# Performance work log

Measured on AMD Instinct MI355X. Metric: run time of the kernel, lower is better.

The kernel has to match this reference:

```python
import jax, jax.numpy as jnp
import numpy as np

N = 50000
E = 400000
IN_DIM = 256
H1 = 512
H2 = 128
P_DROP = 0.5


def setup_inputs() -> dict:
    key = jax.random.key(0)
    ks = jax.random.split(key, 8)
    x = jax.random.normal(ks[0], (N, IN_DIM), dtype=jnp.float32)
    edge_index = jax.random.randint(ks[1], (2, E), 0, N, dtype=jnp.int64)
    W1 = jax.random.normal(ks[2], (IN_DIM, H1), dtype=jnp.float32) * (1.0 / np.sqrt(IN_DIM))
    b1 = jnp.zeros((H1,), dtype=jnp.float32)
    W2 = jax.random.normal(ks[3], (H1, H2), dtype=jnp.float32) * (1.0 / np.sqrt(H1))
    b2 = jnp.zeros((H2,), dtype=jnp.float32)
    a = jnp.full((1,), 0.25, dtype=jnp.float32)  # PReLU default init
    mask1 = jax.random.bernoulli(ks[4], 1.0 - P_DROP, (N, H1))
    mask2 = jax.random.bernoulli(ks[5], 1.0 - P_DROP, (N, H2))
    return {"x": x, "edge_index": edge_index, "W1": W1, "b1": b1,
            "W2": W2, "b2": b2, "a": a, "mask1": mask1, "mask2": mask2}


def reference(x, edge_index, W1, b1, W2, b2, a, mask1, mask2):
    n = x.shape[0]
    loop = jnp.arange(n, dtype=edge_index.dtype)
    src = jnp.concatenate([edge_index[0], loop])  # [E+N] with self-loops
    dst = jnp.concatenate([edge_index[1], loop])
    # symmetric normalization: deg^-1/2[src] * deg^-1/2[dst]
    deg = jax.ops.segment_sum(jnp.ones(src.shape[0], x.dtype), dst, num_segments=n)
    dis = jnp.where(deg > 0, jax.lax.rsqrt(jnp.maximum(deg, 1.0)), 0.0)
    norm = dis[src] * dis[dst]  # [E+N]

    scale = 1.0 / (1.0 - P_DROP)

    def gcn_conv(h, W, b):
        h = h @ W                               # dense transform [n, out]
        msg = h[src] * norm[:, None]            # gather + normalize [E+N, out]
        return jax.ops.segment_sum(msg, dst, num_segments=n) + b

    def prelu_dropout(h, mask):
        h = jnp.where(h >= 0, h, a * h)         # PReLU (shared scalar a)
        return jnp.where(mask, h * scale, 0.0)  # dropout p=0.5

    feat1 = prelu_dropout(gcn_conv(x, W1, b1), mask1)
    feat2 = prelu_dropout(gcn_conv(feat1, W2, b2), mask2)
    return feat2
```

## Files before the change

kernel.cpp:

```cpp
#include <hip/hip_runtime.h>
#include <hip/hip_bf16.h>

#define IN_DIM 256
#define H1 512
#define H2 128
#define BM 128
#define SCAN_CHUNK 4096

typedef unsigned short u16;
typedef unsigned long long u64;
typedef __attribute__((ext_vector_type(8))) short short8;
typedef __attribute__((ext_vector_type(4))) float floatx4;

__device__ __forceinline__ u16 f2bf(float f) {
    union { float f; unsigned u; } c; c.f = f;
    unsigned u = c.u;
    return (u16)((u + 0x7fffu + ((u >> 16) & 1u)) >> 16);
}
__device__ __forceinline__ float bflo(unsigned w) {
    union { unsigned u; float f; } c; c.u = w << 16; return c.f;
}
__device__ __forceinline__ float bfhi(unsigned w) {
    union { unsigned u; float f; } c; c.u = w & 0xffff0000u; return c.f;
}


__global__ __launch_bounds__(256) void prep_kernel(const int4* __restrict__ mask4,
        u64* __restrict__ bits, int total4,
        const int* __restrict__ dstA, int* __restrict__ counts, int E, int n,
        const float* __restrict__ W1, u16* __restrict__ w1t,
        const float* __restrict__ W2, u16* __restrict__ w2t,
        int PB, int HB, int T1B) {
    int b = blockIdx.x;
    if (b < PB) {
        int gid = b * 256 + threadIdx.x;
        int lane = threadIdx.x & 63;
        int4 v = (gid < total4) ? mask4[gid] : make_int4(0, 0, 0, 0);
        u64 b0 = __ballot(v.x != 0);
        u64 b1 = __ballot(v.y != 0);
        u64 b2 = __ballot(v.z != 0);
        u64 b3 = __ballot(v.w != 0);
        u64 sel = (lane == 0) ? b0 : (lane == 1) ? b1 : (lane == 2) ? b2 : b3;
        if (lane < 4 && gid < total4)
            bits[(size_t)(gid >> 6) * 4 + lane] = sel;
    } else if (b < PB + HB) {
        int e = (b - PB) * 256 + threadIdx.x;
        if (e < E) {
            int d = dstA[e];
            if ((unsigned)d < (unsigned)n) atomicAdd(&counts[d], 1);
        }
    } else if (b < PB + HB + T1B) {
        int idx = (b - PB - HB) * 256 + threadIdx.x;
        if (idx < IN_DIM * H1) {
            int k = idx >> 9, c = idx & (H1 - 1);
            w1t[c * IN_DIM + k] = f2bf(W1[idx]);
        }
    } else {
        int idx = (b - PB - HB - T1B) * 256 + threadIdx.x;
        if (idx < H1 * H2) {
            int k = idx >> 7, c = idx & (H2 - 1);
            w2t[c * H1 + k] = f2bf(W2[idx]);
        }
    }
}


__global__ __launch_bounds__(256) void partial_sum_kernel(const int* __restrict__ counts,
        int* __restrict__ partials, int n) {
    int t = threadIdx.x;
    int base = blockIdx.x * SCAN_CHUNK + t * 16;
    int s = 0;
    int m = (base < n) ? min(16, n - base) : 0;
    for (int i = 0; i < m; ++i) s += (counts[base + i] + 1) & ~1;
    __shared__ int red[256];
    red[t] = s;
    __syncthreads();
    for (int off = 128; off > 0; off >>= 1) {
        if (t < off) red[t] += red[t + off];
        __syncthreads();
    }
    if (t == 0) partials[blockIdx.x] = red[0];
}

__global__ void scan_partials_kernel(int* __restrict__ partials, int nb,
                                     unsigned* __restrict__ ts_zero_row) {
    int t = threadIdx.x;
    if (t < 64) ts_zero_row[t] = 0;
    if (t == 0 && blockIdx.x == 0) {
        int run = 0;
        for (int i = 0; i < nb; ++i) { int c = partials[i]; partials[i] = run; run += c; }
        partials[nb] = run;
    }
}

__global__ __launch_bounds__(256) void scan_emit_kernel(const int* __restrict__ counts,
        const int* __restrict__ partials, int* __restrict__ row_start,
        int* __restrict__ cursor, float* __restrict__ dis,
        int* __restrict__ csr, int n, int nb) {
    int t = threadIdx.x;
    int base = blockIdx.x * SCAN_CHUNK + t * 16;
    int cnt[16];
    int s = 0;
    int m = (base < n) ? min(16, n - base) : 0;
    for (int i = 0; i < m; ++i) { cnt[i] = counts[base + i]; s += (cnt[i] + 1) & ~1; }
    __shared__ int red[256];
    red[t] = s;
    __syncthreads();
    for (int off = 1; off < 256; off <<= 1) {
        int v = red[t];
        int vo = (t >= off) ? red[t - off] : 0;
        __syncthreads();
        red[t] = v + vo;
        __syncthreads();
    }
    int run = partials[blockIdx.x] + (t ? red[t - 1] : 0);
    for (int i = 0; i < m; ++i) {
        int c = cnt[i];
        row_start[base + i] = run;
        cursor[base + i] = run;
        dis[base + i] = rsqrtf((float)(c + 1));
        if (c & 1) csr[run + c] = n;
        run += (c + 1) & ~1;
    }
    if (blockIdx.x == 0 && t == 0) row_start[n] = partials[nb];
}

__global__ void scatter_kernel(const int* __restrict__ srcA, const int* __restrict__ dstA,
                               int* __restrict__ cursor, int* __restrict__ csr,
                               int E, int n) {
    int e = blockIdx.x * blockDim.x + threadIdx.x;
    if (e < E) {
        int d = dstA[e];
        int s = srcA[e];
        if ((unsigned)d < (unsigned)n && (unsigned)s < (unsigned)n) {
            int p = atomicAdd(&cursor[d], 1);
            csr[p] = s;
        }
    }
}

__global__ void scale_cast_kernel(const float* __restrict__ x, const float* __restrict__ dis,
                                  u16* __restrict__ xs, int n) {
    int gid = blockIdx.x * blockDim.x + threadIdx.x;
    int total = (n + 1) * (IN_DIM / 4);
    if (gid >= total) return;
    int node = gid >> 6;
    uint2 o = make_uint2(0, 0);
    if (node < n) {
        float4 v = ((const float4*)x)[gid];
        float d = dis[node];
        o.x = (unsigned)f2bf(v.x * d) | ((unsigned)f2bf(v.y * d) << 16);
        o.y = (unsigned)f2bf(v.z * d) | ((unsigned)f2bf(v.w * d) << 16);
    }
    ((uint2*)xs)[gid] = o;
}


__global__ __launch_bounds__(256) void agg1_kernel(const u16* __restrict__ xs,
        const int* __restrict__ row_start, const int* __restrict__ csr,
        const float* __restrict__ dis, u16* __restrict__ aggx, int n) {
    int gid = blockIdx.x * blockDim.x + threadIdx.x;
    int w = gid >> 6, lane = gid & 63;
    if (w >= n) return;
    const uint4* base = (const uint4*)xs;
    int half = lane >> 5, hl = lane & 31;
    float a0 = 0.f, a1 = 0.f, a2 = 0.f, a3 = 0.f, a4 = 0.f, a5 = 0.f, a6 = 0.f, a7 = 0.f;
    if (half == 0) {
        uint4 u = base[(size_t)w * 32 + hl];
        a0 = bflo(u.x); a1 = bfhi(u.x); a2 = bflo(u.y); a3 = bfhi(u.y);
        a4 = bflo(u.z); a5 = bfhi(u.z); a6 = bflo(u.w); a7 = bfhi(u.w);
    }
    int b = row_start[w], e = row_start[w + 1];
    int i = b;
    for (; i + 8 <= e; i += 8) {
        int s0 = csr[i + half],     s1 = csr[i + 2 + half];
        int s2 = csr[i + 4 + half], s3 = csr[i + 6 + half];
        uint4 u0 = base[(size_t)s0 * 32 + hl];
        uint4 u1 = base[(size_t)s1 * 32 + hl];
        uint4 u2 = base[(size_t)s2 * 32 + hl];
        uint4 u3 = base[(size_t)s3 * 32 + hl];
        a0 += (bflo(u0.x) + bflo(u1.x)) + (bflo(u2.x) + bflo(u3.x));
        a1 += (bfhi(u0.x) + bfhi(u1.x)) + (bfhi(u2.x) + bfhi(u3.x));
        a2 += (bflo(u0.y) + bflo(u1.y)) + (bflo(u2.y) + bflo(u3.y));
        a3 += (bfhi(u0.y) + bfhi(u1.y)) + (bfhi(u2.y) + bfhi(u3.y));
        a4 += (bflo(u0.z) + bflo(u1.z)) + (bflo(u2.z) + bflo(u3.z));
        a5 += (bfhi(u0.z) + bfhi(u1.z)) + (bfhi(u2.z) + bfhi(u3.z));
        a6 += (bflo(u0.w) + bflo(u1.w)) + (bflo(u2.w) + bflo(u3.w));
        a7 += (bfhi(u0.w) + bfhi(u1.w)) + (bfhi(u2.w) + bfhi(u3.w));
    }
    for (; i < e; i += 2) {
        int s = csr[i + half];
        uint4 u = base[(size_t)s * 32 + hl];
        a0 += bflo(u.x); a1 += bfhi(u.x); a2 += bflo(u.y); a3 += bfhi(u.y);
        a4 += bflo(u.z); a5 += bfhi(u.z); a6 += bflo(u.w); a7 += bfhi(u.w);
    }
    a0 += __shfl_xor(a0, 32); a1 += __shfl_xor(a1, 32);
    a2 += __shfl_xor(a2, 32); a3 += __shfl_xor(a3, 32);
    a4 += __shfl_xor(a4, 32); a5 += __shfl_xor(a5, 32);
    a6 += __shfl_xor(a6, 32); a7 += __shfl_xor(a7, 32);
    if (half == 0) {
        float dd = dis[w];
        uint4 o;
        o.x = (unsigned)f2bf(a0 * dd) | ((unsigned)f2bf(a1 * dd) << 16);
        o.y = (unsigned)f2bf(a2 * dd) | ((unsigned)f2bf(a3 * dd) << 16);
        o.z = (unsigned)f2bf(a4 * dd) | ((unsigned)f2bf(a5 * dd) << 16);
        o.w = (unsigned)f2bf(a6 * dd) | ((unsigned)f2bf(a7 * dd) << 16);
        ((uint4*)aggx)[(size_t)w * 32 + hl] = o;
    }
}


__global__ __launch_bounds__(256) void gemm1_kernel(const u16* __restrict__ A,
        const u16* __restrict__ Bt, const float* __restrict__ bias,
        const float* __restrict__ a_p, const u64* __restrict__ mbits,
        u16* __restrict__ out, int M) {
    const int K = IN_DIM;
    __shared__ u64 mb[BM * 5];
    int tid = threadIdx.x;
    int wave = tid >> 6, lane = tid & 63;
    int quad = lane >> 4, l16 = lane & 15;
    int wm = wave & 1, wn = wave >> 1;
    int m0 = blockIdx.x * BM, n0 = blockIdx.y * BM;

    for (int u = tid; u < BM * 4; u += 256) {
        int row = u >> 2, j = u & 3;
        int gr = m0 + row;
        u64 val = 0;
        if (gr < M) val = mbits[(size_t)gr * 8 + (n0 >> 8) * 4 + j];
        mb[row * 5 + j] = val;
    }

    floatx4 acc[4][4];
#pragma unroll
    for (int i = 0; i < 4; i++)
#pragma unroll
        for (int j = 0; j < 4; j++) acc[i][j] = (floatx4){0.f, 0.f, 0.f, 0.f};

    const u16* aptr[4];
#pragma unroll
    for (int mt = 0; mt < 4; mt++) {
        int row = m0 + wm * 64 + mt * 16 + l16;
        if (row >= M) row = M - 1;
        aptr[mt] = A + (size_t)row * K + quad * 8;
    }
    const u16* bptr[4];
#pragma unroll
    for (int i = 0; i < 4; i++)
        bptr[i] = Bt + (size_t)(n0 + wn * 64 + i * 16 + l16) * K + quad * 8;

#pragma unroll
    for (int k0 = 0; k0 < K; k0 += 64) {
        short8 bf[4][2];
#pragma unroll
        for (int i = 0; i < 4; i++) {
            bf[i][0] = *(const short8*)(bptr[i] + k0);
            bf[i][1] = *(const short8*)(bptr[i] + k0 + 32);
        }
#pragma unroll
        for (int mt = 0; mt < 4; mt++) {
            short8 af0 = *(const short8*)(aptr[mt] + k0);
            short8 af1 = *(const short8*)(aptr[mt] + k0 + 32);
#pragma unroll
            for (int nt = 0; nt < 4; nt++) {
                acc[mt][nt] = __builtin_amdgcn_mfma_f32_16x16x32_bf16(
                    af0, bf[nt][0], acc[mt][nt], 0, 0, 0);
                acc[mt][nt] = __builtin_amdgcn_mfma_f32_16x16x32_bf16(
                    af1, bf[nt][1], acc[mt][nt], 0, 0, 0);
            }
        }
    }

    __syncthreads();
    float alpha = a_p[0];
#pragma unroll
    for (int mt = 0; mt < 4; mt++) {
#pragma unroll
        for (int r = 0; r < 4; r++) {
            int lr = wm * 64 + mt * 16 + quad * 4 + r;
            int row = m0 + lr;
            if (row >= M) continue;
#pragma unroll
            for (int nt = 0; nt < 4; nt++) {
                int c64 = nt * 16 + l16;
                int col = n0 + wn * 64 + c64;
                float v = acc[mt][nt][r] + bias[col];
                v = (v >= 0.f) ? v : alpha * v;
                u64 w = mb[lr * 5 + (l16 & 3)];
                int bit = ((n0 >> 2) + wn * 16 + nt * 4 + (l16 >> 2)) & 63;
                v = ((w >> bit) & 1ull) ? v * 2.0f : 0.0f;
                out[(size_t)row * H1 + col] = f2bf(v);
            }
        }
    }
}


__global__ __launch_bounds__(256) void gemm2_kernel(const u16* __restrict__ A,
        const u16* __restrict__ Bt, const float* __restrict__ dis,
        u16* __restrict__ out, int M) {
    const int K = H1;
    int tid = threadIdx.x;
    int wave = tid >> 6, lane = tid & 63;
    int quad = lane >> 4, l16 = lane & 15;
    int wm = wave & 1, wn = wave >> 1;
    int m0 = blockIdx.x * 64;

    floatx4 acc[2][4];
#pragma unroll
    for (int i = 0; i < 2; i++)
#pragma unroll
        for (int j = 0; j < 4; j++) acc[i][j] = (floatx4){0.f, 0.f, 0.f, 0.f};

    const u16* aptr[2];
#pragma unroll
    for (int mt = 0; mt < 2; mt++) {
        int row = m0 + wm * 32 + mt * 16 + l16;
        if (row >= M) row = M - 1;
        aptr[mt] = A + (size_t)row * K + quad * 8;
    }
    const u16* bptr[4];
#pragma unroll
    for (int i = 0; i < 4; i++)
        bptr[i] = Bt + (size_t)(wn * 64 + i * 16 + l16) * K + quad * 8;

#pragma unroll 2
    for (int k0 = 0; k0 < K; k0 += 64) {
        short8 bf[4][2];
#pragma unroll
        for (int i = 0; i < 4; i++) {
            bf[i][0] = *(const short8*)(bptr[i] + k0);
            bf[i][1] = *(const short8*)(bptr[i] + k0 + 32);
        }
#pragma unroll
        for (int mt = 0; mt < 2; mt++) {
            short8 af0 = *(const short8*)(aptr[mt] + k0);
            short8 af1 = *(const short8*)(aptr[mt] + k0 + 32);
#pragma unroll
            for (int nt = 0; nt < 4; nt++) {
                acc[mt][nt] = __builtin_amdgcn_mfma_f32_16x16x32_bf16(
                    af0, bf[nt][0], acc[mt][nt], 0, 0, 0);
                acc[mt][nt] = __builtin_amdgcn_mfma_f32_16x16x32_bf16(
                    af1, bf[nt][1], acc[mt][nt], 0, 0, 0);
            }
        }
    }

#pragma unroll
    for (int mt = 0; mt < 2; mt++) {
#pragma unroll
        for (int r = 0; r < 4; r++) {
            int row = m0 + wm * 32 + mt * 16 + quad * 4 + r;
            if (row >= M) continue;
            float dd = dis[row];
#pragma unroll
            for (int nt = 0; nt < 4; nt++) {
                int col = wn * 64 + nt * 16 + l16;
                out[(size_t)row * H2 + col] = f2bf(acc[mt][nt][r] * dd);
            }
        }
    }
}


__global__ __launch_bounds__(256) void agg2_kernel(const u16* __restrict__ ts,
        const int* __restrict__ row_start, const int* __restrict__ csr,
        const float* __restrict__ dis, const float* __restrict__ b2,
        const float* __restrict__ a_p, const int* __restrict__ mask,
        float* __restrict__ out, int n) {
    int gid = blockIdx.x * blockDim.x + threadIdx.x;
    int w = gid >> 6, lane = gid & 63;
    if (w >= n) return;
    const uint2* base = (const uint2*)ts;
    int half = lane >> 5, hl = lane & 31;
    float a0 = 0.f, a1 = 0.f, a2 = 0.f, a3 = 0.f;
    if (half == 0) {
        uint2 u = base[(size_t)w * 32 + hl];
        a0 = bflo(u.x); a1 = bfhi(u.x); a2 = bflo(u.y); a3 = bfhi(u.y);
    }
    int b = row_start[w], e = row_start[w + 1];
    int i = b;
    for (; i + 8 <= e; i += 8) {
        int s0 = csr[i + half],     s1 = csr[i + 2 + half];
        int s2 = csr[i + 4 + half], s3 = csr[i + 6 + half];
        uint2 u0 = base[(size_t)s0 * 32 + hl];
        uint2 u1 = base[(size_t)s1 * 32 + hl];
        uint2 u2 = base[(size_t)s2 * 32 + hl];
        uint2 u3 = base[(size_t)s3 * 32 + hl];
        a0 += (bflo(u0.x) + bflo(u1.x)) + (bflo(u2.x) + bflo(u3.x));
        a1 += (bfhi(u0.x) + bfhi(u1.x)) + (bfhi(u2.x) + bfhi(u3.x));
        a2 += (bflo(u0.y) + bflo(u1.y)) + (bflo(u2.y) + bflo(u3.y));
        a3 += (bfhi(u0.y) + bfhi(u1.y)) + (bfhi(u2.y) + bfhi(u3.y));
    }
    for (; i < e; i += 2) {
        int s = csr[i + half];
        uint2 u = base[(size_t)s * 32 + hl];
        a0 += bflo(u.x); a1 += bfhi(u.x); a2 += bflo(u.y); a3 += bfhi(u.y);
    }
    a0 += __shfl_xor(a0, 32); a1 += __shfl_xor(a1, 32);
    a2 += __shfl_xor(a2, 32); a3 += __shfl_xor(a3, 32);
    if (half == 0) {
        float dd = dis[w];
        float alpha = a_p[0];
        float4 bb = ((const float4*)b2)[hl];
        float v0 = dd * a0 + bb.x;
        float v1 = dd * a1 + bb.y;
        float v2 = dd * a2 + bb.z;
        float v3 = dd * a3 + bb.w;
        v0 = (v0 >= 0.f) ? v0 : alpha * v0;
        v1 = (v1 >= 0.f) ? v1 : alpha * v1;
        v2 = (v2 >= 0.f) ? v2 : alpha * v2;
        v3 = (v3 >= 0.f) ? v3 : alpha * v3;
        int4 m = ((const int4*)mask)[(size_t)w * 32 + hl];
        v0 = m.x ? v0 * 2.f : 0.f;
        v1 = m.y ? v1 * 2.f : 0.f;
        v2 = m.z ? v2 * 2.f : 0.f;
        v3 = m.w ? v3 * 2.f : 0.f;
        ((float4*)out)[(size_t)w * 32 + hl] = make_float4(v0, v1, v2, v3);
    }
}


extern "C" void kernel_launch(void* const* d_in, const int* in_sizes, int n_in,
                              void* d_out, int out_size, void* d_ws, size_t ws_size,
                              hipStream_t stream) {
    const float* x  = (const float*)d_in[0];
    const int* ei   = (const int*)d_in[1];
    const float* W1 = (const float*)d_in[2];
    const float* b1 = (const float*)d_in[3];
    const float* W2 = (const float*)d_in[4];
    const float* b2 = (const float*)d_in[5];
    const float* ap = (const float*)d_in[6];
    const int* mask1 = (const int*)d_in[7];
    const int* mask2 = (const int*)d_in[8];

    int n = in_sizes[0] / IN_DIM;
    int E = in_sizes[1] / 2;
    const int* srcA = ei;
    const int* dstA = ei + E;

    char* p = (char*)d_ws;
    auto alloc = [&](size_t bytes) {
        char* r = p;
        p += (bytes + 255) & ~(size_t)255;
        return r;
    };
    u16* feat1     = (u16*)alloc((size_t)n * H1 * 2);
    u16* xs        = feat1;
    u16* ts        = (u16*)alloc((size_t)(n + 1) * H2 * 2);
    u64* bits1     = (u64*)ts;
    u16* w1t       = (u16*)alloc((size_t)IN_DIM * H1 * 2);
    u16* w2t       = (u16*)alloc((size_t)H1 * H2 * 2);
    float* dis     = (float*)alloc((size_t)n * 4);
    int* counts    = (int*)alloc((size_t)n * 4);
    int* cursor    = (int*)alloc((size_t)n * 4);
    int* row_start = (int*)alloc(((size_t)n + 1) * 4);
    int* csr       = (int*)alloc(((size_t)E + n + 64) * 4);
    int nscan = (n + SCAN_CHUNK - 1) / SCAN_CHUNK;
    int* partials  = (int*)alloc(((size_t)nscan + 1) * 4);
    u16* aggx      = (u16*)d_out;
    if ((size_t)(p - (char*)d_ws) > ws_size) return;

    const int tpb = 256;
    int total4 = n * H1 / 4;
    int PB = (total4 + tpb - 1) / tpb;
    int HB = (E + tpb - 1) / tpb;
    int T1B = (IN_DIM * H1 + tpb - 1) / tpb;
    int T2B = (H1 * H2 + tpb - 1) / tpb;
    hipMemsetAsync(counts, 0, (size_t)n * 4, stream);
    prep_kernel<<<PB + HB + T1B + T2B, tpb, 0, stream>>>((const int4*)mask1, bits1, total4,
        dstA, counts, E, n, W1, w1t, W2, w2t, PB, HB, T1B);
    partial_sum_kernel<<<nscan, tpb, 0, stream>>>(counts, partials, n);
    scan_partials_kernel<<<1, 64, 0, stream>>>(partials, nscan,
        (unsigned*)(ts + (size_t)n * H2));
    scan_emit_kernel<<<nscan, tpb, 0, stream>>>(counts, partials, row_start, cursor, dis,
                                                csr, n, nscan);
    scatter_kernel<<<(E + tpb - 1) / tpb, tpb, 0, stream>>>(srcA, dstA, cursor, csr, E, n);
    scale_cast_kernel<<<(((n + 1) * (IN_DIM / 4)) + tpb - 1) / tpb, tpb, 0, stream>>>(x, dis, xs, n);
    agg1_kernel<<<(n * 64 + tpb - 1) / tpb, tpb, 0, stream>>>(xs, row_start, csr, dis, aggx, n);
    dim3 g1((n + BM - 1) / BM, H1 / BM);
    gemm1_kernel<<<g1, tpb, 0, stream>>>(aggx, w1t, b1, ap, bits1, feat1, n);
    dim3 g2((n + 63) / 64, 1);
    gemm2_kernel<<<g2, tpb, 0, stream>>>(feat1, w2t, dis, ts, n);
    agg2_kernel<<<(n * 64 + tpb - 1) / tpb, tpb, 0, stream>>>(ts, row_start, csr, dis, b2, ap,
                                                              mask2, (float*)d_out, n);
}
```

Measured before the change: 450.6 us.

## Fuse layer-1 GEMM epilogue with layer-2 GEMM via shared-memory tile

Replaces the separate gemm1 and gemm2 kernels with one kernel per 64-row tile. The aggregated input tile is staged in LDS, the 512-wide hidden layer is computed in two 256-column halves with PReLU and dropout applied, and each half is fed straight into the second GEMM from LDS. This removes the write and re-read of the n×512 bf16 feat1 intermediate and one launch. The cost is lower parallelism (one block per 64 rows), extra syncs, and repeated W1/W2 reads from global memory per block. Buffers are reallocated so the mask bits and xs no longer alias feat1 or ts.

```diff
diff --git a/kernel.cpp b/kernel.cpp
--- a/kernel.cpp
+++ b/kernel.cpp
@@ -4,7 +4,7 @@
 #define IN_DIM 256
 #define H1 512
 #define H2 128
-#define BM 128
+#define LDA 264
 #define SCAN_CHUNK 4096
 
 typedef unsigned short u16;
@@ -210,154 +210,120 @@
 }
 
 
-__global__ __launch_bounds__(256) void gemm1_kernel(const u16* __restrict__ A,
-        const u16* __restrict__ Bt, const float* __restrict__ bias,
+__global__ __launch_bounds__(256) void gemm_fused_kernel(const u16* __restrict__ A,
+        const u16* __restrict__ W1t, const float* __restrict__ b1,
         const float* __restrict__ a_p, const u64* __restrict__ mbits,
-        u16* __restrict__ out, int M) {
-    const int K = IN_DIM;
-    __shared__ u64 mb[BM * 5];
+        const u16* __restrict__ W2t, const float* __restrict__ dis,
+        u16* __restrict__ ts, int M) {
+    __shared__ __align__(16) u16 As[64 * LDA];
+    __shared__ __align__(16) u16 Fs[64 * LDA];
+    __shared__ u64 Mb[64 * 9];
     int tid = threadIdx.x;
     int wave = tid >> 6, lane = tid & 63;
     int quad = lane >> 4, l16 = lane & 15;
-    int wm = wave & 1, wn = wave >> 1;
-    int m0 = blockIdx.x * BM, n0 = blockIdx.y * BM;
-
-    for (int u = tid; u < BM * 4; u += 256) {
-        int row = u >> 2, j = u & 3;
+    int m0 = blockIdx.x * 64;
+
+    for (int u = tid; u < 2048; u += 256) {
+        int row = u >> 5, seg = u & 31;
+        uint4 av = make_uint4(0, 0, 0, 0);
         int gr = m0 + row;
-        u64 val = 0;
-        if (gr < M) val = mbits[(size_t)gr * 8 + (n0 >> 8) * 4 + j];
-        mb[row * 5 + j] = val;
-    }
-
-    floatx4 acc[4][4];
-#pragma unroll
-    for (int i = 0; i < 4; i++)
-#pragma unroll
-        for (int j = 0; j < 4; j++) acc[i][j] = (floatx4){0.f, 0.f, 0.f, 0.f};
-
-    const u16* aptr[4];
-#pragma unroll
-    for (int mt = 0; mt < 4; mt++) {
-        int row = m0 + wm * 64 + mt * 16 + l16;
-        if (row >= M) row = M - 1;
-        aptr[mt] = A + (size_t)row * K + quad * 8;
-    }
-    const u16* bptr[4];
-#pragma unroll
-    for (int i = 0; i < 4; i++)
-        bptr[i] = Bt + (size_t)(n0 + wn * 64 + i * 16 + l16) * K + quad * 8;
-
-#pragma unroll
-    for (int k0 = 0; k0 < K; k0 += 64) {
-        short8 bf[4][2];
-#pragma unroll
-        for (int i = 0; i < 4; i++) {
-            bf[i][0] = *(const short8*)(bptr[i] + k0);
-            bf[i][1] = *(const short8*)(bptr[i] + k0 + 32);
-        }
+        if (gr < M) av = *(const uint4*)&A[(size_t)gr * IN_DIM + seg * 8];
+        *(uint4*)&As[row * LDA + seg * 8] = av;
+    }
+    for (int u = tid; u < 512; u += 256) {
+        int row = u >> 3, j = u & 7;
+        int gr = m0 + row;
+        Mb[row * 9 + j] = (gr < M) ? mbits[(size_t)gr * 8 + j] : 0;
+    }
+    __syncthreads();
+
+    floatx4 acc2[8];
+#pragma unroll
+    for (int i = 0; i < 8; i++) acc2[i] = (floatx4){0.f, 0.f, 0.f, 0.f};
+    float alpha = a_p[0];
+
+#pragma unroll
+    for (int h = 0; h < 2; h++) {
+        floatx4 acc1[4][4];
+#pragma unroll
+        for (int i = 0; i < 4; i++)
+#pragma unroll
+            for (int j = 0; j < 4; j++) acc1[i][j] = (floatx4){0.f, 0.f, 0.f, 0.f};
+        const u16* bptr1[4];
+#pragma unroll
+        for (int nt = 0; nt < 4; nt++)
+            bptr1[nt] = W1t + (size_t)(h * 256 + wave * 64 + nt * 16 + l16) * IN_DIM + quad * 8;
+        float bias_v[4];
+#pragma unroll
+        for (int nt = 0; nt < 4; nt++)
+            bias_v[nt] = b1[h * 256 + wave * 64 + nt * 16 + l16];
+#pragma unroll
+        for (int k0 = 0; k0 < 256; k0 += 64) {
+            short8 bf[4][2], af[4][2];
+#pragma unroll
+            for (int nt = 0; nt < 4; nt++) {
+                bf[nt][0] = *(const short8*)(bptr1[nt] + k0);
+                bf[nt][1] = *(const short8*)(bptr1[nt] + k0 + 32);
+            }
+#pragma unroll
+            for (int mt = 0; mt < 4; mt++) {
+                af[mt][0] = *(const short8*)&As[(mt * 16 + l16) * LDA + k0 + quad * 8];
+                af[mt][1] = *(const short8*)&As[(mt * 16 + l16) * LDA + k0 + 32 + quad * 8];
+            }
+#pragma unroll
+            for (int mt = 0; mt < 4; mt++)
+#pragma unroll
+                for (int nt = 0; nt < 4; nt++) {
+                    acc1[mt][nt] = __builtin_amdgcn_mfma_f32_16x16x32_bf16(
+                        af[mt][0], bf[nt][0], acc1[mt][nt], 0, 0, 0);
+                    acc1[mt][nt] = __builtin_amdgcn_mfma_f32_16x16x32_bf16(
+                        af[mt][1], bf[nt][1], acc1[mt][nt], 0, 0, 0);
+                }
+        }
+
+        __syncthreads();
 #pragma unroll
         for (int mt = 0; mt < 4; mt++) {
-            short8 af0 = *(const short8*)(aptr[mt] + k0);
-            short8 af1 = *(const short8*)(aptr[mt] + k0 + 32);
-#pragma unroll
-            for (int nt = 0; nt < 4; nt++) {
-                acc[mt][nt] = __builtin_amdgcn_mfma_f32_16x16x32_bf16(
-                    af0, bf[nt][0], acc[mt][nt], 0, 0, 0);
-                acc[mt][nt] = __builtin_amdgcn_mfma_f32_16x16x32_bf16(
-                    af1, bf[nt][1], acc[mt][nt], 0, 0, 0);
+#pragma unroll
+            for (int r = 0; r < 4; r++) {
+                int row_l = mt * 16 + quad * 4 + r;
+#pragma unroll
+                for (int nt = 0; nt < 4; nt++) {
+                    int col_l = wave * 64 + nt * 16 + l16;
+                    float v = acc1[mt][nt][r] + bias_v[nt];
+                    v = (v >= 0.f) ? v : alpha * v;
+                    u64 wbits = Mb[row_l * 9 + h * 4 + (l16 & 3)];
+                    int bit = wave * 16 + nt * 4 + (l16 >> 2);
+                    v = ((wbits >> bit) & 1ull) ? v * 2.0f : 0.0f;
+                    Fs[row_l * LDA + col_l] = f2bf(v);
+                }
             }
         }
-    }
-
-    __syncthreads();
-    float alpha = a_p[0];
-#pragma unroll
-    for (int mt = 0; mt < 4; mt++) {
-#pragma unroll
-        for (int r = 0; r < 4; r++) {
-            int lr = wm * 64 + mt * 16 + quad * 4 + r;
-            int row = m0 + lr;
-            if (row >= M) continue;
-#pragma unroll
-            for (int nt = 0; nt < 4; nt++) {
-                int c64 = nt * 16 + l16;
-                int col = n0 + wn * 64 + c64;
-                float v = acc[mt][nt][r] + bias[col];
-                v = (v >= 0.f) ? v : alpha * v;
-                u64 w = mb[lr * 5 + (l16 & 3)];
-                int bit = ((n0 >> 2) + wn * 16 + nt * 4 + (l16 >> 2)) & 63;
-                v = ((w >> bit) & 1ull) ? v * 2.0f : 0.0f;
-                out[(size_t)row * H1 + col] = f2bf(v);
-            }
-        }
-    }
-}
-
-
-__global__ __launch_bounds__(256) void gemm2_kernel(const u16* __restrict__ A,
-        const u16* __restrict__ Bt, const float* __restrict__ dis,
-        u16* __restrict__ out, int M) {
-    const int K = H1;
-    int tid = threadIdx.x;
-    int wave = tid >> 6, lane = tid & 63;
-    int quad = lane >> 4, l16 = lane & 15;
-    int wm = wave & 1, wn = wave >> 1;
-    int m0 = blockIdx.x * 64;
-
-    floatx4 acc[2][4];
-#pragma unroll
-    for (int i = 0; i < 2; i++)
-#pragma unroll
-        for (int j = 0; j < 4; j++) acc[i][j] = (floatx4){0.f, 0.f, 0.f, 0.f};
-
-    const u16* aptr[2];
-#pragma unroll
-    for (int mt = 0; mt < 2; mt++) {
-        int row = m0 + wm * 32 + mt * 16 + l16;
-        if (row >= M) row = M - 1;
-        aptr[mt] = A + (size_t)row * K + quad * 8;
-    }
-    const u16* bptr[4];
-#pragma unroll
-    for (int i = 0; i < 4; i++)
-        bptr[i] = Bt + (size_t)(wn * 64 + i * 16 + l16) * K + quad * 8;
-
-#pragma unroll 2
-    for (int k0 = 0; k0 < K; k0 += 64) {
-        short8 bf[4][2];
-#pragma unroll
-        for (int i = 0; i < 4; i++) {
-            bf[i][0] = *(const short8*)(bptr[i] + k0);
-            bf[i][1] = *(const short8*)(bptr[i] + k0 + 32);
-        }
-#pragma unroll
-        for (int mt = 0; mt < 2; mt++) {
-            short8 af0 = *(const short8*)(aptr[mt] + k0);
-            short8 af1 = *(const short8*)(aptr[mt] + k0 + 32);
-#pragma unroll
-            for (int nt = 0; nt < 4; nt++) {
-                acc[mt][nt] = __builtin_amdgcn_mfma_f32_16x16x32_bf16(
-                    af0, bf[nt][0], acc[mt][nt], 0, 0, 0);
-                acc[mt][nt] = __builtin_amdgcn_mfma_f32_16x16x32_bf16(
-                    af1, bf[nt][1], acc[mt][nt], 0, 0, 0);
-            }
-        }
-    }
-
-#pragma unroll
-    for (int mt = 0; mt < 2; mt++) {
-#pragma unroll
-        for (int r = 0; r < 4; r++) {
-            int row = m0 + wm * 32 + mt * 16 + quad * 4 + r;
-            if (row >= M) continue;
-            float dd = dis[row];
-#pragma unroll
-            for (int nt = 0; nt < 4; nt++) {
-                int col = wn * 64 + nt * 16 + l16;
-                out[(size_t)row * H2 + col] = f2bf(acc[mt][nt][r] * dd);
-            }
-        }
+        __syncthreads();
+
+        const u16* bptr2 = W2t + (size_t)l16 * H1 + h * 256 + quad * 8;
+#pragma unroll
+        for (int k0 = 0; k0 < 256; k0 += 32) {
+            short8 af2 = *(const short8*)&Fs[(wave * 16 + l16) * LDA + k0 + quad * 8];
+            short8 bf2[8];
+#pragma unroll
+            for (int nt2 = 0; nt2 < 8; nt2++)
+                bf2[nt2] = *(const short8*)(bptr2 + (size_t)nt2 * 16 * H1 + k0);
+#pragma unroll
+            for (int nt2 = 0; nt2 < 8; nt2++)
+                acc2[nt2] = __builtin_amdgcn_mfma_f32_16x16x32_bf16(
+                    af2, bf2[nt2], acc2[nt2], 0, 0, 0);
+        }
+    }
+
+#pragma unroll
+    for (int r = 0; r < 4; r++) {
+        int row = m0 + wave * 16 + quad * 4 + r;
+        if (row >= M) continue;
+        float dd = dis[row];
+#pragma unroll
+        for (int nt2 = 0; nt2 < 8; nt2++)
+            ts[(size_t)row * H2 + nt2 * 16 + l16] = f2bf(acc2[nt2][r] * dd);
     }
 }
 
@@ -444,10 +410,9 @@
         p += (bytes + 255) & ~(size_t)255;
         return r;
     };
-    u16* feat1     = (u16*)alloc((size_t)n * H1 * 2);
-    u16* xs        = feat1;
+    u16* xs        = (u16*)alloc((size_t)(n + 1) * IN_DIM * 2);
     u16* ts        = (u16*)alloc((size_t)(n + 1) * H2 * 2);
-    u64* bits1     = (u64*)ts;
+    u64* bits1     = (u64*)alloc((size_t)n * (H1 / 64) * 8);
     u16* w1t       = (u16*)alloc((size_t)IN_DIM * H1 * 2);
     u16* w2t       = (u16*)alloc((size_t)H1 * H2 * 2);
     float* dis     = (float*)alloc((size_t)n * 4);
@@ -477,10 +442,8 @@
     scatter_kernel<<<(E + tpb - 1) / tpb, tpb, 0, stream>>>(srcA, dstA, cursor, csr, E, n);
     scale_cast_kernel<<<(((n + 1) * (IN_DIM / 4)) + tpb - 1) / tpb, tpb, 0, stream>>>(x, dis, xs, n);
     agg1_kernel<<<(n * 64 + tpb - 1) / tpb, tpb, 0, stream>>>(xs, row_start, csr, dis, aggx, n);
-    dim3 g1((n + BM - 1) / BM, H1 / BM);
-    gemm1_kernel<<<g1, tpb, 0, stream>>>(aggx, w1t, b1, ap, bits1, feat1, n);
-    dim3 g2((n + 63) / 64, 1);
-    gemm2_kernel<<<g2, tpb, 0, stream>>>(feat1, w2t, dis, ts, n);
+    gemm_fused_kernel<<<(n + 63) / 64, tpb, 0, stream>>>(aggx, w1t, b1, ap, bits1,
+                                                         w2t, dis, ts, n);
     agg2_kernel<<<(n * 64 + tpb - 1) / tpb, tpb, 0, stream>>>(ts, row_start, csr, dis, b2, ap,
                                                               mask2, (float*)d_out, n);
 }
```

Result: faster. 436.9 us (-3.1%).
